# Kernel optimization log

Hardware: AMD Instinct MI355X
Metric: run time of the kernel (lower is better)

The kernel has to match this reference:

```python
import jax, jax.numpy as jnp
import numpy as np

N = 50000      # nodes
E = 800000     # random edges (self-loops added in reference, as PyG GATConv does)
G = 1024       # graphs in the batch
F_IN = 35      # num_features_xd
H1, C1 = 10, 35   # gcn1: heads=10, out=35 -> concat 350
H2, C2 = 1, 128   # gcn2: heads=1, out=128
NEG_SLOPE = 0.2   # PyG GATConv default leaky_relu slope


def setup_inputs() -> dict:
    key = jax.random.key(0)
    ks = jax.random.split(key, 16)
    g = lambda k, sh, fan: jax.random.normal(k, sh, jnp.float32) / jnp.sqrt(jnp.float32(fan))
    return {
        "x": jax.random.normal(ks[0], (N, F_IN), jnp.float32),
        "edge_index": jax.random.randint(ks[1], (2, E), 0, N),
        "batch": jnp.sort(jax.random.randint(ks[2], (N,), 0, G)),
        # gcn1 params
        "W1": g(ks[3], (F_IN, H1 * C1), F_IN),
        "att_src1": g(ks[4], (H1, C1), C1),
        "att_dst1": g(ks[5], (H1, C1), C1),
        "b1": jnp.zeros((H1 * C1,), jnp.float32),
        # gcn2 params
        "W2": g(ks[6], (H1 * C1, H2 * C2), H1 * C1),
        "att_src2": g(ks[7], (H2, C2), C2),
        "att_dst2": g(ks[8], (H2, C2), C2),
        "b2": jnp.zeros((H2 * C2,), jnp.float32),
        # dense head
        "Wg": g(ks[9], (C2, C2), C2),
        "bg": jnp.zeros((C2,), jnp.float32),
        "Wo": g(ks[10], (C2, 1), C2),
        "bo": jnp.zeros((1,), jnp.float32),
    }


def _gat_conv(x, src, dst, W, att_src, att_dst, b, heads, ch):
    """PyG GATConv (eval mode): edge attention + segment softmax + scatter sum."""
    h = (x @ W).reshape(-1, heads, ch)                      # [N,H,C]
    a_s = jnp.einsum('nhc,hc->nh', h, att_src)              # [N,H]
    a_d = jnp.einsum('nhc,hc->nh', h, att_dst)
    e = jax.nn.leaky_relu(a_s[src] + a_d[dst], NEG_SLOPE)   # [Etot,H]
    m = jax.ops.segment_max(e, dst, num_segments=N)         # segment softmax over dst
    ex = jnp.exp(e - m[dst])
    den = jax.ops.segment_sum(ex, dst, num_segments=N)
    alpha = ex / den[dst]                                   # [Etot,H]
    out = jax.ops.segment_sum(alpha[:, :, None] * h[src], dst, num_segments=N)
    return out.reshape(-1, heads * ch) + b                  # concat heads + bias


def reference(x, edge_index, batch, W1, att_src1, att_dst1, b1,
              W2, att_src2, att_dst2, b2, Wg, bg, Wo, bo):
    # add self-loops (PyG GATConv default add_self_loops=True)
    loop = jnp.arange(N, dtype=edge_index.dtype)
    src = jnp.concatenate([edge_index[0], loop])
    dst = jnp.concatenate([edge_index[1], loop])

    h = jax.nn.elu(_gat_conv(x, src, dst, W1, att_src1, att_dst1, b1, H1, C1))
    h = jax.nn.relu(_gat_conv(h, src, dst, W2, att_src2, att_dst2, b2, H2, C2))

    # global max pool over graphs
    pooled = jax.ops.segment_max(h, batch, num_segments=G)
    pooled = jnp.where(jnp.isneginf(pooled), 0.0, pooled)   # guard empty graphs

    z = jax.nn.relu(pooled @ Wg + bg)
    return z @ Wo + bo                                      # [G, 1]
```

## Files before the change

kernel.cpp:

```cpp
#include <hip/hip_runtime.h>
#include <hip/hip_bf16.h>
#include <cmath>

#define N_NODES 50000
#define N_EDGES 800000
#define N_GRAPHS 1024
#define F_IN 35
#define H1 10
#define C1 35
#define HC1 350
#define C2 128
#define NB256 196

typedef unsigned int uint32;
typedef __attribute__((ext_vector_type(8))) short short8;
typedef __attribute__((ext_vector_type(4))) float f32x4;

static __device__ __forceinline__ float bflo(uint32 u) { return __uint_as_float(u << 16); }
static __device__ __forceinline__ float bfhi(uint32 u) { return __uint_as_float(u & 0xffff0000u); }
static __device__ __forceinline__ unsigned short bfbits(float f) {
    return __builtin_bit_cast(unsigned short, __float2bfloat16(f));
}
static __device__ __forceinline__ uint32 packbf(float a, float b) {
    return ((uint32)bfbits(b) << 16) | (uint32)bfbits(a);
}
static __device__ __forceinline__ float lrelu(float e) { return (e > 0.f) ? e : 0.2f * e; }

__global__ void k_count(const int* __restrict__ dst, int* __restrict__ deg) {
    int e = blockIdx.x * blockDim.x + threadIdx.x;
    if (e < N_EDGES) atomicAdd(&deg[dst[e]], 1);
}

__global__ __launch_bounds__(256) void k_bsum(const int* __restrict__ deg, int* __restrict__ bsum) {
    const int i = blockIdx.x * 256 + threadIdx.x;
    int v = (i < N_NODES) ? deg[i] : 0;
#pragma unroll
    for (int off = 32; off; off >>= 1) v += __shfl_xor(v, off);
    __shared__ int ws[4];
    if ((threadIdx.x & 63) == 0) ws[threadIdx.x >> 6] = v;
    __syncthreads();
    if (threadIdx.x == 0) bsum[blockIdx.x] = ws[0] + ws[1] + ws[2] + ws[3];
}

__global__ __launch_bounds__(256) void k_bscan(const int* __restrict__ bsum, int* __restrict__ bpre) {
    __shared__ int buf[256];
    const int t = threadIdx.x;
    int v = (t < NB256) ? bsum[t] : 0;
    buf[t] = v;
    __syncthreads();
    for (int off = 1; off < 256; off <<= 1) {
        int u = (t >= off) ? buf[t - off] : 0;
        __syncthreads();
        buf[t] += u;
        __syncthreads();
    }
    if (t < NB256) bpre[t] = buf[t] - v;
}

__global__ __launch_bounds__(256) void k_boffs(const int* __restrict__ deg,
                                               const int* __restrict__ bpre,
                                               int* __restrict__ offs, int* __restrict__ cursor) {
    const int b = blockIdx.x, t = threadIdx.x;
    const int i = b * 256 + t;
    const int lane = t & 63, wid = t >> 6;
    int v = (i < N_NODES) ? deg[i] : 0;
    int s = v;
#pragma unroll
    for (int off = 1; off < 64; off <<= 1) {
        int u = __shfl_up(s, off);
        if (lane >= off) s += u;
    }
    __shared__ int wsum[4];
    if (lane == 63) wsum[wid] = s;
    __syncthreads();
    int wbase = 0;
    for (int w = 0; w < wid; ++w) wbase += wsum[w];
    int excl = bpre[b] + wbase + s - v;
    if (i < N_NODES) { offs[i] = excl; cursor[i] = excl; }
    if (i == 0) offs[N_NODES] = N_EDGES;
}

__global__ void k_fill(const int* __restrict__ src, const int* __restrict__ dst,
                       int* __restrict__ cursor, int* __restrict__ csr) {
    int e = blockIdx.x * blockDim.x + threadIdx.x;
    if (e < N_EDGES) {
        int p = atomicAdd(&cursor[dst[e]], 1);
        csr[p] = src[e];
    }
}

#define XBLK ((N_NODES * 8 + 255) / 256)
__global__ __launch_bounds__(256) void k_prep(const float* __restrict__ x,
                                              const float* __restrict__ W1,
                                              const float* __restrict__ attS1,
                                              const float* __restrict__ attD1,
                                              const float* __restrict__ W2,
                                              uint32* __restrict__ xbf,
                                              uint32* __restrict__ W1f,
                                              uint32* __restrict__ W2f) {
    const int b = blockIdx.x, t = threadIdx.x;
    if (b < XBLK) {
        int idx = b * 256 + t;
        if (idx >= N_NODES * 8) return;
        int n = idx >> 3, tt = idx & 7;
        uint32 o[4];
#pragma unroll
        for (int p = 0; p < 4; ++p) {
            int k0 = tt * 8 + 2 * p;
            float a = (k0 < F_IN) ? x[(size_t)n * F_IN + k0] : 0.f;
            float bb = (k0 + 1 < F_IN) ? x[(size_t)n * F_IN + k0 + 1] : 0.f;
            o[p] = packbf(a, bb);
        }
        uint32* d = xbf + (size_t)n * 32 + tt * 4;
        d[0] = o[0]; d[1] = o[1]; d[2] = o[2]; d[3] = o[3];
    } else if (b < XBLK + 12) {
        int idx = (b - XBLK) * 256 + t;
        if (idx >= 2 * 24 * 64) return;
        int lane = idx & 63;
        int tt = (idx >> 6) % 24;
        int kk = idx / (24 * 64);
        int c = tt * 16 + (lane & 15);
        int k0 = kk * 32 + (lane >> 4) * 8;
        uint32 o[4];
#pragma unroll
        for (int jj = 0; jj < 4; ++jj) {
            float v[2];
#pragma unroll
            for (int half = 0; half < 2; ++half) {
                int k = k0 + 2 * jj + half;
                float val = 0.f;
                if (k < F_IN) {
                    if (c < HC1) {
                        val = W1[k * HC1 + c];
                    } else if (c >= 352 && c < 362) {
                        int h = c - 352;
                        float s = 0.f;
                        for (int cc = 0; cc < C1; ++cc)
                            s = fmaf(W1[k * HC1 + h * C1 + cc], attS1[h * C1 + cc], s);
                        val = s;
                    } else if (c >= 368 && c < 378) {
                        int h = c - 368;
                        float s = 0.f;
                        for (int cc = 0; cc < C1; ++cc)
                            s = fmaf(W1[k * HC1 + h * C1 + cc], attD1[h * C1 + cc], s);
                        val = s;
                    }
                }
                v[half] = val;
            }
            o[jj] = packbf(v[0], v[1]);
        }
        uint32* d = W1f + (size_t)idx * 4;
        d[0] = o[0]; d[1] = o[1]; d[2] = o[2]; d[3] = o[3];
    } else {
        int idx = (b - XBLK - 12) * 256 + t;
        if (idx >= 11 * 8 * 64) return;
        int lane = idx & 63;
        int tt = (idx >> 6) & 7;
        int kk = idx >> 9;
        int c = tt * 16 + (lane & 15);
        int k0 = kk * 32 + (lane >> 4) * 8;
        uint32 o[4];
#pragma unroll
        for (int jj = 0; jj < 4; ++jj) {
            int ka = k0 + 2 * jj, kb = ka + 1;
            float va = (ka < HC1) ? W2[ka * C2 + c] : 0.f;
            float vb = (kb < HC1) ? W2[kb * C2 + c] : 0.f;
            o[jj] = packbf(va, vb);
        }
        uint32* d = W2f + (size_t)idx * 4;
        d[0] = o[0]; d[1] = o[1]; d[2] = o[2]; d[3] = o[3];
    }
}

__global__ __launch_bounds__(256) void k_gemm1(const short* __restrict__ xbf,
                                               const short8* __restrict__ W1f,
                                               unsigned short* __restrict__ h1b,
                                               float* __restrict__ a_s1,
                                               float* __restrict__ a_d1) {
    const int lane = threadIdx.x & 63;
    const int wid = threadIdx.x >> 6;
    const int mtile = blockIdx.x * 4 + wid;
    if (mtile >= N_NODES / 16) return;
    const int c_lo = lane & 15, grp = lane >> 4;
    const int m0 = mtile * 16;
    const short* aptr = xbf + (size_t)(m0 + c_lo) * 64 + grp * 8;

    f32x4 acc[24];
#pragma unroll
    for (int t = 0; t < 24; ++t) acc[t] = (f32x4){0.f, 0.f, 0.f, 0.f};
#pragma unroll
    for (int kk = 0; kk < 2; ++kk) {
        short8 a = *reinterpret_cast<const short8*>(aptr + kk * 32);
#pragma unroll
        for (int t = 0; t < 24; ++t) {
            short8 b = W1f[(kk * 24 + t) * 64 + lane];
            acc[t] = __builtin_amdgcn_mfma_f32_16x16x32_bf16(a, b, acc[t], 0, 0, 0);
        }
    }
#pragma unroll
    for (int r = 0; r < 4; ++r) {
        int node = m0 + grp * 4 + r;
#pragma unroll
        for (int t = 0; t < 22; ++t)
            h1b[(size_t)node * 352 + t * 16 + c_lo] = bfbits(acc[t][r]);
        if (c_lo < 10) {
            a_s1[node * 10 + c_lo] = acc[22][r];
            a_d1[node * 10 + c_lo] = acc[23][r];
        }
    }
}

__global__ __launch_bounds__(256) void k_agg1(const uint4* __restrict__ feat4,
                                              const float* __restrict__ a_s,
                                              const float* __restrict__ a_d,
                                              const int* __restrict__ offs,
                                              const int* __restrict__ csr,
                                              const float* __restrict__ bias,
                                              uint4* __restrict__ x2p4) {
    __shared__ float al[4][10][72];
    __shared__ float rdn[4][10];
    __shared__ int totmax[4];
    const int tid = threadIdx.x;
    const int lane = tid & 63, wid = tid >> 6;
    const int d = blockIdx.x * 4 + wid;
    const int o0 = offs[d];
    const int deg = offs[d + 1] - o0;
    const int total = deg + 1;
    const int cl = lane & 15, g = lane >> 4;

    if (lane < 8) {
#pragma unroll
        for (int h = 0; h < 10; ++h) al[wid][h][64 + lane] = 0.f;
    }
    if (lane == 0) totmax[wid] = total;
    __syncthreads();
    const int tmx = max(max(totmax[0], totmax[1]), max(totmax[2], totmax[3]));
    const int rounds = (tmx + 63) >> 6;

    float add[10];
    {
        const float2* ap = (const float2*)(a_d + (size_t)d * 10);
#pragma unroll
        for (int p = 0; p < 5; ++p) { float2 v = ap[p]; add[2 * p] = v.x; add[2 * p + 1] = v.y; }
    }
    const int u0 = cl, u1 = cl + 16, u2 = cl + 32;
    const bool has2 = (u2 < 44);
    const int hLo0 = (8 * u0) / 35, hHi0 = min((8 * u0 + 7) / 35, 9), bnd0 = 35 * hHi0;
    const int hLo1 = (8 * u1) / 35, hHi1 = min((8 * u1 + 7) / 35, 9), bnd1 = 35 * hHi1;
    const int hLo2 = has2 ? (8 * u2) / 35 : 0, hHi2 = has2 ? min((8 * u2 + 7) / 35, 9) : 0;
    const int bnd2 = 35 * hHi2;

    float acc0[8], acc1[8], acc2[8];
#pragma unroll
    for (int q = 0; q < 8; ++q) { acc0[q] = 0.f; acc1[q] = 0.f; acc2[q] = 0.f; }
    float den[10];
#pragma unroll
    for (int h = 0; h < 10; ++h) den[h] = 0.f;

    for (int rb = 0; rb < rounds; ++rb) {
        const int base = rb << 6;
        const int i = base + lane;
        int s_mine = d;
        if (i < total) {
            s_mine = (i < deg) ? csr[o0 + i] : d;
            const float2* ap = (const float2*)(a_s + (size_t)s_mine * 10);
            float2 v0 = ap[0], v1 = ap[1], v2 = ap[2], v3 = ap[3], v4 = ap[4];
            float e;
#define DOH(h, val)                            \
            e = __expf(lrelu((val) + add[h])); \
            den[h] += e;                       \
            al[wid][h][lane] = e;
            DOH(0, v0.x) DOH(1, v0.y) DOH(2, v1.x) DOH(3, v1.y) DOH(4, v2.x)
            DOH(5, v2.y) DOH(6, v3.x) DOH(7, v3.y) DOH(8, v4.x) DOH(9, v4.y)
#undef DOH
        } else {
#pragma unroll
            for (int h = 0; h < 10; ++h) al[wid][h][lane] = 0.f;
        }
        __syncthreads();
        const int cnt = min(64, total - base);
        if (cnt > 0) {
            int scur = __shfl(s_mine, g);
            uint4 v0 = feat4[(size_t)scur * 44 + u0];
            uint4 v1 = feat4[(size_t)scur * 44 + u1];
            uint4 v2 = has2 ? feat4[(size_t)scur * 44 + u2] : (uint4){0, 0, 0, 0};
            for (int jb = 0; jb < cnt; jb += 4) {
                uint4 w0 = v0, w1 = v1, w2 = v2;
                const int jj = jb + g;
                if (jb + 4 < cnt) {
                    int sn = __shfl(s_mine, jb + 4 + g);
                    v0 = feat4[(size_t)sn * 44 + u0];
                    v1 = feat4[(size_t)sn * 44 + u1];
                    if (has2) v2 = feat4[(size_t)sn * 44 + u2];
                }
#define ACCSLOT(ACC, W, HLO, HHI, BND, U)                                   \
                {                                                           \
                    float aLo = al[wid][HLO][jj], aHi = al[wid][HHI][jj];   \
                    _Pragma("unroll")                                       \
                    for (int q = 0; q < 4; ++q) {                           \
                        uint32 u = (q == 0) ? W.x : (q == 1) ? W.y : (q == 2) ? W.z : W.w; \
                        float aA = (8 * (U) + 2 * q >= (BND)) ? aHi : aLo;  \
                        float aB = (8 * (U) + 2 * q + 1 >= (BND)) ? aHi : aLo; \
                        ACC[2 * q] = fmaf(aA, bflo(u), ACC[2 * q]);         \
                        ACC[2 * q + 1] = fmaf(aB, bfhi(u), ACC[2 * q + 1]); \
                    }                                                       \
                }
                ACCSLOT(acc0, w0, hLo0, hHi0, bnd0, u0)
                ACCSLOT(acc1, w1, hLo1, hHi1, bnd1, u1)
                if (has2) ACCSLOT(acc2, w2, hLo2, hHi2, bnd2, u2)
#undef ACCSLOT
            }
        }
        __syncthreads();
    }
#pragma unroll
    for (int q = 0; q < 8; ++q) {
        acc0[q] += __shfl_xor(acc0[q], 16); acc0[q] += __shfl_xor(acc0[q], 32);
        acc1[q] += __shfl_xor(acc1[q], 16); acc1[q] += __shfl_xor(acc1[q], 32);
        acc2[q] += __shfl_xor(acc2[q], 16); acc2[q] += __shfl_xor(acc2[q], 32);
    }
#pragma unroll
    for (int off = 32; off > 0; off >>= 1) {
#pragma unroll
        for (int h = 0; h < 10; ++h) den[h] += __shfl_xor(den[h], off);
    }
    if (lane == 0) {
#pragma unroll
        for (int h = 0; h < 10; ++h) rdn[wid][h] = 1.f / den[h];
    }
    __syncthreads();
    if (g == 0) {
#define EPI(ACC, HLO, HHI, BND, U)                                          \
        {                                                                   \
            float rLo = rdn[wid][HLO], rHi = rdn[wid][HHI];                 \
            uint32 o[4];                                                    \
            _Pragma("unroll")                                               \
            for (int q = 0; q < 4; ++q) {                                   \
                int p = 4 * (U) + q;                                        \
                if (p < 175) {                                              \
                    int ch0 = 8 * (U) + 2 * q;                              \
                    float rA = (ch0 >= (BND)) ? rHi : rLo;                  \
                    float rB = (ch0 + 1 >= (BND)) ? rHi : rLo;              \
                    float v0 = ACC[2 * q] * rA + bias[ch0];                 \
                    float v1 = ACC[2 * q + 1] * rB + bias[ch0 + 1];         \
                    v0 = (v0 > 0.f) ? v0 : expm1f(v0);                      \
                    v1 = (v1 > 0.f) ? v1 : expm1f(v1);                      \
                    o[q] = packbf(v0, v1);                                  \
                } else {                                                    \
                    o[q] = 0u;                                              \
                }                                                           \
            }                                                               \
            uint4 ov = {o[0], o[1], o[2], o[3]};                            \
            x2p4[(size_t)d * 44 + (U)] = ov;                                \
        }
        EPI(acc0, hLo0, hHi0, bnd0, u0)
        EPI(acc1, hLo1, hHi1, bnd1, u1)
        if (has2) EPI(acc2, hLo2, hHi2, bnd2, u2)
#undef EPI
    }
}

__global__ __launch_bounds__(256) void k_gemm2(const short* __restrict__ x2p,
                                               const short8* __restrict__ W2f,
                                               const float* __restrict__ attS,
                                               const float* __restrict__ attD,
                                               unsigned short* __restrict__ h2b,
                                               float* __restrict__ a_s2, float* __restrict__ a_d2) {
    const int lane = threadIdx.x & 63;
    const int wid = threadIdx.x >> 6;
    const int mtile = blockIdx.x * 4 + wid;
    if (mtile >= N_NODES / 16) return;
    const int c_lo = lane & 15, grp = lane >> 4;
    const int m0 = mtile * 16;
    const short* aptr = x2p + (size_t)(m0 + c_lo) * 352 + grp * 8;

    f32x4 acc[8];
#pragma unroll
    for (int t = 0; t < 8; ++t) acc[t] = (f32x4){0.f, 0.f, 0.f, 0.f};
#pragma unroll
    for (int kk = 0; kk < 11; ++kk) {
        short8 a = *reinterpret_cast<const short8*>(aptr + kk * 32);
#pragma unroll
        for (int t = 0; t < 8; ++t) {
            short8 b = W2f[(kk * 8 + t) * 64 + lane];
            acc[t] = __builtin_amdgcn_mfma_f32_16x16x32_bf16(a, b, acc[t], 0, 0, 0);
        }
    }
    float attSv[8], attDv[8];
#pragma unroll
    for (int t = 0; t < 8; ++t) {
        attSv[t] = attS[t * 16 + c_lo];
        attDv[t] = attD[t * 16 + c_lo];
    }
    float ps[4] = {0, 0, 0, 0}, pd[4] = {0, 0, 0, 0};
#pragma unroll
    for (int t = 0; t < 8; ++t)
#pragma unroll
        for (int r = 0; r < 4; ++r) {
            ps[r] = fmaf(acc[t][r], attSv[t], ps[r]);
            pd[r] = fmaf(acc[t][r], attDv[t], pd[r]);
        }
#pragma unroll
    for (int r = 0; r < 4; ++r) {
        int node = m0 + grp * 4 + r;
#pragma unroll
        for (int t = 0; t < 8; ++t) h2b[(size_t)node * C2 + t * 16 + c_lo] = bfbits(acc[t][r]);
    }
#pragma unroll
    for (int r = 0; r < 4; ++r) {
        float s = ps[r], dd = pd[r];
#pragma unroll
        for (int off = 1; off < 16; off <<= 1) {
            s += __shfl_xor(s, off);
            dd += __shfl_xor(dd, off);
        }
        if (c_lo == 0) {
            int node = m0 + grp * 4 + r;
            a_s2[node] = s;
            a_d2[node] = dd;
        }
    }
}

__global__ __launch_bounds__(256) void k_agg2(const uint4* __restrict__ feat4,
                                              const float* __restrict__ a_s,
                                              const float* __restrict__ a_d,
                                              const int* __restrict__ offs,
                                              const int* __restrict__ csr,
                                              const float* __restrict__ b2,
                                              float* __restrict__ out2) {
    const int lane = threadIdx.x & 63;
    const int wid = threadIdx.x >> 6;
    const int d = blockIdx.x * 4 + wid;
    const int o0 = offs[d];
    const int deg = offs[d + 1] - o0;
    const int total = deg + 1;
    const float add = a_d[d];
    const int g = lane >> 4, cl = lane & 15;

    float acc[8];
#pragma unroll
    for (int q = 0; q < 8; ++q) acc[q] = 0.f;
    float den = 0.f;

    for (int base = 0; base < total; base += 64) {
        const int i = base + lane;
        int s_mine = d;
        float e_mine = 0.f;
        if (i < total) {
            s_mine = (i < deg) ? csr[o0 + i] : d;
            e_mine = __expf(lrelu(a_s[s_mine] + add));
            den += e_mine;
        }
        const int cnt = min(64, total - base);
        int sj = __shfl(s_mine, g);
        float aj = __shfl(e_mine, g);
        uint4 vc = feat4[(size_t)sj * 16 + cl];
        for (int jb = 0; jb < cnt; jb += 4) {
            uint4 v = vc;
            float a = aj;
            if (jb + 4 < cnt) {
                int ni = jb + 4 + g;
                int sn = __shfl(s_mine, ni);
                aj = __shfl(e_mine, ni);
                vc = feat4[(size_t)sn * 16 + cl];
            }
            acc[0] = fmaf(a, bflo(v.x), acc[0]);
            acc[1] = fmaf(a, bfhi(v.x), acc[1]);
            acc[2] = fmaf(a, bflo(v.y), acc[2]);
            acc[3] = fmaf(a, bfhi(v.y), acc[3]);
            acc[4] = fmaf(a, bflo(v.z), acc[4]);
            acc[5] = fmaf(a, bfhi(v.z), acc[5]);
            acc[6] = fmaf(a, bflo(v.w), acc[6]);
            acc[7] = fmaf(a, bfhi(v.w), acc[7]);
        }
    }
#pragma unroll
    for (int q = 0; q < 8; ++q) {
        acc[q] += __shfl_xor(acc[q], 16);
        acc[q] += __shfl_xor(acc[q], 32);
    }
#pragma unroll
    for (int off = 32; off > 0; off >>= 1) den += __shfl_xor(den, off);

    if (lane < 16) {
        const float rden = 1.f / den;
        const float4* bp = (const float4*)(b2 + 8 * cl);
        float4 b0 = bp[0], b1 = bp[1];
        float4 o0v, o1v;
        o0v.x = fmaxf(acc[0] * rden + b0.x, 0.f);
        o0v.y = fmaxf(acc[1] * rden + b0.y, 0.f);
        o0v.z = fmaxf(acc[2] * rden + b0.z, 0.f);
        o0v.w = fmaxf(acc[3] * rden + b0.w, 0.f);
        o1v.x = fmaxf(acc[4] * rden + b1.x, 0.f);
        o1v.y = fmaxf(acc[5] * rden + b1.y, 0.f);
        o1v.z = fmaxf(acc[6] * rden + b1.z, 0.f);
        o1v.w = fmaxf(acc[7] * rden + b1.w, 0.f);
        float4* op = (float4*)(out2 + (size_t)d * C2 + 8 * cl);
        op[0] = o0v;
        op[1] = o1v;
    }
}

__global__ __launch_bounds__(128) void k_pool(const float* __restrict__ out2,
                                              const int* __restrict__ batch,
                                              float* __restrict__ pooled) {
    const int c = threadIdx.x;
    const int n0 = blockIdx.x * 50;
    const int n1 = min(n0 + 50, N_NODES);
    int curB = batch[n0];
    float curM = 0.f;
    float v = out2[(size_t)n0 * C2 + c];
    for (int n = n0; n < n1; ++n) {
        float cur = v;
        int b = batch[n];
        if (n + 1 < n1) v = out2[(size_t)(n + 1) * C2 + c];
        if (b != curB) {
            atomicMax((int*)&pooled[curB * C2 + c], __float_as_int(curM));
            curB = b;
            curM = cur;
        } else {
            curM = fmaxf(curM, cur);
        }
    }
    atomicMax((int*)&pooled[curB * C2 + c], __float_as_int(curM));
}

__global__ __launch_bounds__(128) void k_head(const float* __restrict__ pooled,
                                              const float* __restrict__ Wg,
                                              const float* __restrict__ bg,
                                              const float* __restrict__ Wo,
                                              const float* __restrict__ bo,
                                              float* __restrict__ out) {
    __shared__ float p[C2];
    __shared__ float wsum[2];
    const int g = blockIdx.x;
    const int tid = threadIdx.x;
    p[tid] = pooled[g * C2 + tid];
    __syncthreads();
    float acc = bg[tid];
#pragma unroll 8
    for (int k = 0; k < C2; ++k) acc = fmaf(p[k], Wg[k * C2 + tid], acc);
    float z = fmaxf(acc, 0.f);
    float prod = z * Wo[tid];
#pragma unroll
    for (int off = 32; off; off >>= 1) prod += __shfl_down(prod, off);
    if ((tid & 63) == 0) wsum[tid >> 6] = prod;
    __syncthreads();
    if (tid == 0) out[g] = wsum[0] + wsum[1] + bo[0];
}

extern "C" void kernel_launch(void* const* d_in, const int* in_sizes, int n_in,
                              void* d_out, int out_size, void* d_ws, size_t ws_size,
                              hipStream_t stream) {
    const float* x        = (const float*)d_in[0];
    const int*   ei       = (const int*)d_in[1];
    const int*   batch    = (const int*)d_in[2];
    const float* W1       = (const float*)d_in[3];
    const float* att_src1 = (const float*)d_in[4];
    const float* att_dst1 = (const float*)d_in[5];
    const float* b1       = (const float*)d_in[6];
    const float* W2       = (const float*)d_in[7];
    const float* att_src2 = (const float*)d_in[8];
    const float* att_dst2 = (const float*)d_in[9];
    const float* b2       = (const float*)d_in[10];
    const float* Wg       = (const float*)d_in[11];
    const float* bg       = (const float*)d_in[12];
    const float* Wo       = (const float*)d_in[13];
    const float* bo       = (const float*)d_in[14];
    const int* src = ei;
    const int* dst = ei + N_EDGES;

    char* ws = (char*)d_ws;
    size_t off = 0;
    auto alloc = [&](size_t bytes) -> char* {
        char* p = ws + off;
        off = (off + bytes + 255) & ~(size_t)255;
        return p;
    };
    int*    deg    = (int*)alloc((size_t)N_NODES * 4);
    int*    offs   = (int*)alloc((size_t)(N_NODES + 1) * 4);
    int*    cursor = (int*)alloc((size_t)N_NODES * 4);
    int*    csr    = (int*)alloc((size_t)N_EDGES * 4);
    int*    bsum   = (int*)alloc((size_t)NB256 * 4);
    int*    bpre   = (int*)alloc((size_t)NB256 * 4);
    float*  a_s1   = (float*)alloc((size_t)N_NODES * H1 * 4);
    float*  a_d1   = (float*)alloc((size_t)N_NODES * H1 * 4);
    float*  a_s2   = (float*)alloc((size_t)N_NODES * 4);
    float*  a_d2   = (float*)alloc((size_t)N_NODES * 4);
    float*  pooled = (float*)alloc((size_t)N_GRAPHS * C2 * 4);
    uint32* xbf    = (uint32*)alloc((size_t)N_NODES * 32 * 4);
    unsigned short* h1b = (unsigned short*)alloc((size_t)N_NODES * 352 * 2);
    uint32* x2p    = (uint32*)alloc((size_t)N_NODES * 176 * 4);
    unsigned short* h2b = (unsigned short*)alloc((size_t)N_NODES * C2 * 2);
    uint32* W1f    = (uint32*)alloc((size_t)2 * 24 * 64 * 16);
    uint32* W2f    = (uint32*)alloc((size_t)11 * 8 * 64 * 16);
    float*  out2   = (float*)h1b;

    hipMemsetAsync(deg, 0, (size_t)N_NODES * 4, stream);
    hipMemsetAsync(pooled, 0, (size_t)N_GRAPHS * C2 * 4, stream);

    k_count<<<(N_EDGES + 255) / 256, 256, 0, stream>>>(dst, deg);
    k_bsum<<<NB256, 256, 0, stream>>>(deg, bsum);
    k_bscan<<<1, 256, 0, stream>>>(bsum, bpre);
    k_boffs<<<NB256, 256, 0, stream>>>(deg, bpre, offs, cursor);
    k_fill<<<(N_EDGES + 255) / 256, 256, 0, stream>>>(src, dst, cursor, csr);

    k_prep<<<XBLK + 34, 256, 0, stream>>>(x, W1, att_src1, att_dst1, W2, xbf, W1f, W2f);

    k_gemm1<<<(N_NODES / 16 + 3) / 4, 256, 0, stream>>>((const short*)xbf, (const short8*)W1f,
                                                        h1b, a_s1, a_d1);

    k_agg1<<<N_NODES / 4, 256, 0, stream>>>((const uint4*)h1b, a_s1, a_d1, offs, csr, b1,
                                            (uint4*)x2p);

    k_gemm2<<<(N_NODES / 16 + 3) / 4, 256, 0, stream>>>((const short*)x2p, (const short8*)W2f,
                                                        att_src2, att_dst2, h2b, a_s2, a_d2);

    k_agg2<<<N_NODES / 4, 256, 0, stream>>>((const uint4*)h2b, a_s2, a_d2, offs, csr, b2, out2);

    k_pool<<<(N_NODES + 49) / 50, 128, 0, stream>>>(out2, batch, pooled);

    k_head<<<N_GRAPHS, 128, 0, stream>>>(pooled, Wg, bg, Wo, bo, (float*)d_out);
}
```

Measured before the change: 402.4 us.

## Aggregate raw 35-dim inputs per head before layer-1 projection

Layer 1 now uses linearity: instead of projecting every node to 350 channels and then gathering 352-wide bf16 rows per edge, it gathers the 40-wide padded input rows, weights them with per-head attention, and applies the per-head W1 projection afterwards with MFMA. A constant-one input channel carries the bias through the GEMM, and the softmax denominator comes from the aggregated bias channel. Attention logits are computed separately through folded W1·att vectors. This cuts per-edge gather traffic, but it adds a 10×40-per-node intermediate buffer, a larger post-aggregation GEMM, and extra kernels, and it adds occupancy hints.

```diff
diff --git a/kernel.cpp b/kernel.cpp
--- a/kernel.cpp
+++ b/kernel.cpp
@@ -89,36 +89,51 @@
     }
 }
 
-#define XBLK ((N_NODES * 8 + 255) / 256)
+#define XB ((N_NODES * 5 + 255) / 256)
 __global__ __launch_bounds__(256) void k_prep(const float* __restrict__ x,
                                               const float* __restrict__ W1,
                                               const float* __restrict__ attS1,
                                               const float* __restrict__ attD1,
+                                              const float* __restrict__ b1,
                                               const float* __restrict__ W2,
                                               uint32* __restrict__ xbf,
-                                              uint32* __restrict__ W1f,
+                                              float* __restrict__ fold,
+                                              uint32* __restrict__ W1g,
                                               uint32* __restrict__ W2f) {
     const int b = blockIdx.x, t = threadIdx.x;
-    if (b < XBLK) {
+    if (b < XB) {
         int idx = b * 256 + t;
-        if (idx >= N_NODES * 8) return;
-        int n = idx >> 3, tt = idx & 7;
+        if (idx >= N_NODES * 5) return;
+        int n = idx / 5, s = idx - n * 5;
         uint32 o[4];
 #pragma unroll
         for (int p = 0; p < 4; ++p) {
-            int k0 = tt * 8 + 2 * p;
-            float a = (k0 < F_IN) ? x[(size_t)n * F_IN + k0] : 0.f;
-            float bb = (k0 + 1 < F_IN) ? x[(size_t)n * F_IN + k0 + 1] : 0.f;
+            int ch0 = s * 8 + 2 * p, ch1 = ch0 + 1;
+            float a = (ch0 < F_IN) ? x[(size_t)n * F_IN + ch0] : (ch0 == 35 ? 1.f : 0.f);
+            float bb = (ch1 < F_IN) ? x[(size_t)n * F_IN + ch1] : (ch1 == 35 ? 1.f : 0.f);
             o[p] = packbf(a, bb);
         }
-        uint32* d = xbf + (size_t)n * 32 + tt * 4;
+        uint32* d = xbf + (size_t)idx * 4;
         d[0] = o[0]; d[1] = o[1]; d[2] = o[2]; d[3] = o[3];
-    } else if (b < XBLK + 12) {
-        int idx = (b - XBLK) * 256 + t;
-        if (idx >= 2 * 24 * 64) return;
+    } else if (b < XB + 3) {
+        int idx = (b - XB) * 256 + t;
+        if (idx >= 700) return;
+        int k = idx / 20, o = idx - k * 20;
+        int h = (o < 10) ? o : o - 10;
+        const float* att = (o < 10) ? attS1 : attD1;
+        float s = 0.f;
+        for (int c = 0; c < C1; ++c)
+            s = fmaf(W1[k * HC1 + h * C1 + c], att[h * C1 + c], s);
+        fold[k * 20 + o] = s;
+    } else if (b < XB + 3 + 15) {
+        int idx = (b - XB - 3) * 256 + t;
+        if (idx >= 10 * 2 * 3 * 64) return;
         int lane = idx & 63;
-        int tt = (idx >> 6) % 24;
-        int kk = idx / (24 * 64);
+        int rest = idx >> 6;
+        int tt = rest % 3;
+        int rest2 = rest / 3;
+        int kk = rest2 & 1;
+        int h = rest2 >> 1;
         int c = tt * 16 + (lane & 15);
         int k0 = kk * 32 + (lane >> 4) * 8;
         uint32 o[4];
@@ -129,31 +144,18 @@
             for (int half = 0; half < 2; ++half) {
                 int k = k0 + 2 * jj + half;
                 float val = 0.f;
-                if (k < F_IN) {
-                    if (c < HC1) {
-                        val = W1[k * HC1 + c];
-                    } else if (c >= 352 && c < 362) {
-                        int h = c - 352;
-                        float s = 0.f;
-                        for (int cc = 0; cc < C1; ++cc)
-                            s = fmaf(W1[k * HC1 + h * C1 + cc], attS1[h * C1 + cc], s);
-                        val = s;
-                    } else if (c >= 368 && c < 378) {
-                        int h = c - 368;
-                        float s = 0.f;
-                        for (int cc = 0; cc < C1; ++cc)
-                            s = fmaf(W1[k * HC1 + h * C1 + cc], attD1[h * C1 + cc], s);
-                        val = s;
-                    }
+                if (c < C1) {
+                    if (k < F_IN) val = W1[k * HC1 + h * C1 + c];
+                    else if (k == 35) val = b1[h * C1 + c];
                 }
                 v[half] = val;
             }
             o[jj] = packbf(v[0], v[1]);
         }
-        uint32* d = W1f + (size_t)idx * 4;
+        uint32* d = W1g + (size_t)idx * 4;
         d[0] = o[0]; d[1] = o[1]; d[2] = o[2]; d[3] = o[3];
     } else {
-        int idx = (b - XBLK - 12) * 256 + t;
+        int idx = (b - XB - 3 - 15) * 256 + t;
         if (idx >= 11 * 8 * 64) return;
         int lane = idx & 63;
         int tt = (idx >> 6) & 7;
@@ -173,192 +175,173 @@
     }
 }
 
-__global__ __launch_bounds__(256) void k_gemm1(const short* __restrict__ xbf,
-                                               const short8* __restrict__ W1f,
-                                               unsigned short* __restrict__ h1b,
-                                               float* __restrict__ a_s1,
-                                               float* __restrict__ a_d1) {
+__global__ __launch_bounds__(256) void k_att1(const float* __restrict__ x,
+                                              const float* __restrict__ fold,
+                                              float* __restrict__ a_s1,
+                                              float* __restrict__ a_d1) {
+    int idx = blockIdx.x * 256 + threadIdx.x;
+    if (idx >= N_NODES * 20) return;
+    int n = idx / 20, o = idx - n * 20;
+    const float* xr = x + (size_t)n * F_IN;
+    float acc = 0.f;
+#pragma unroll
+    for (int k = 0; k < F_IN; ++k) acc = fmaf(xr[k], fold[k * 20 + o], acc);
+    if (o < 10) a_s1[n * 10 + o] = acc;
+    else        a_d1[n * 10 + (o - 10)] = acc;
+}
+
+__global__ __launch_bounds__(256, 8) void k_aggx(const uint4* __restrict__ xbf4,
+                                                 const float* __restrict__ a_s,
+                                                 const float* __restrict__ a_d,
+                                                 const int* __restrict__ offs,
+                                                 const int* __restrict__ csr,
+                                                 uint4* __restrict__ aggx4) {
+    __shared__ float al[4][10][68];
+    __shared__ float addl[4][10];
+    __shared__ int totmax[4];
+    const int tid = threadIdx.x, lane = tid & 63, wid = tid >> 6;
+    const int d = blockIdx.x * 4 + wid;
+    const int o0 = offs[d];
+    const int deg = offs[d + 1] - o0;
+    const int total = deg + 1;
+    const int g = lane >> 4, u = lane & 15;
+    const int hg = (u >= 10) ? 2 : ((u >= 5) ? 1 : 0);
+    const int sl = u - hg * 5;
+    const bool act = (u < 15);
+    const int h0 = hg * 4;
+
+    if (lane < 10) addl[wid][lane] = a_d[(size_t)d * 10 + lane];
+    if (lane < 4) {
+#pragma unroll
+        for (int h = 0; h < 10; ++h) al[wid][h][64 + lane] = 0.f;
+    }
+    if (lane == 0) totmax[wid] = total;
+    __syncthreads();
+    const int tmx = max(max(totmax[0], totmax[1]), max(totmax[2], totmax[3]));
+    const int rounds = (tmx + 63) >> 6;
+
+    float acc[4][8];
+#pragma unroll
+    for (int a = 0; a < 4; ++a)
+#pragma unroll
+        for (int q = 0; q < 8; ++q) acc[a][q] = 0.f;
+
+    for (int rb = 0; rb < rounds; ++rb) {
+        const int base = rb << 6;
+        const int i = base + lane;
+        int s_mine = d;
+        if (i < total) {
+            if (i < deg) s_mine = csr[o0 + i];
+            const float2* ap = (const float2*)(a_s + (size_t)s_mine * 10);
+            float2 p0 = ap[0], p1 = ap[1], p2 = ap[2], p3 = ap[3], p4 = ap[4];
+            al[wid][0][lane] = __expf(lrelu(p0.x + addl[wid][0]));
+            al[wid][1][lane] = __expf(lrelu(p0.y + addl[wid][1]));
+            al[wid][2][lane] = __expf(lrelu(p1.x + addl[wid][2]));
+            al[wid][3][lane] = __expf(lrelu(p1.y + addl[wid][3]));
+            al[wid][4][lane] = __expf(lrelu(p2.x + addl[wid][4]));
+            al[wid][5][lane] = __expf(lrelu(p2.y + addl[wid][5]));
+            al[wid][6][lane] = __expf(lrelu(p3.x + addl[wid][6]));
+            al[wid][7][lane] = __expf(lrelu(p3.y + addl[wid][7]));
+            al[wid][8][lane] = __expf(lrelu(p4.x + addl[wid][8]));
+            al[wid][9][lane] = __expf(lrelu(p4.y + addl[wid][9]));
+        } else {
+#pragma unroll
+            for (int h = 0; h < 10; ++h) al[wid][h][lane] = 0.f;
+        }
+        __syncthreads();
+        const int cnt = min(64, total - base);
+        if (cnt > 0) {
+            int scur = __shfl(s_mine, g);
+            uint4 v = act ? xbf4[(size_t)scur * 5 + sl] : (uint4){0, 0, 0, 0};
+            for (int jb = 0; jb < cnt; jb += 4) {
+                uint4 w = v;
+                const int jj = jb + g;
+                if (jb + 4 < cnt) {
+                    int sn = __shfl(s_mine, jb + 4 + g);
+                    if (act) v = xbf4[(size_t)sn * 5 + sl];
+                }
+                float f0 = bflo(w.x), f1 = bfhi(w.x), f2 = bflo(w.y), f3 = bfhi(w.y);
+                float f4 = bflo(w.z), f5 = bfhi(w.z), f6 = bflo(w.w), f7 = bfhi(w.w);
+#pragma unroll
+                for (int a = 0; a < 4; ++a) {
+                    const int hidx = min(h0 + a, 9);
+                    const float aj = al[wid][hidx][jj];
+                    acc[a][0] = fmaf(aj, f0, acc[a][0]);
+                    acc[a][1] = fmaf(aj, f1, acc[a][1]);
+                    acc[a][2] = fmaf(aj, f2, acc[a][2]);
+                    acc[a][3] = fmaf(aj, f3, acc[a][3]);
+                    acc[a][4] = fmaf(aj, f4, acc[a][4]);
+                    acc[a][5] = fmaf(aj, f5, acc[a][5]);
+                    acc[a][6] = fmaf(aj, f6, acc[a][6]);
+                    acc[a][7] = fmaf(aj, f7, acc[a][7]);
+                }
+            }
+        }
+        __syncthreads();
+    }
+#pragma unroll
+    for (int a = 0; a < 4; ++a)
+#pragma unroll
+        for (int q = 0; q < 8; ++q) {
+            acc[a][q] += __shfl_xor(acc[a][q], 16);
+            acc[a][q] += __shfl_xor(acc[a][q], 32);
+        }
+    const int nh = (hg == 2) ? 2 : 4;
+#pragma unroll
+    for (int a = 0; a < 4; ++a) {
+        float den = __shfl(acc[a][3], hg * 5 + 4);
+        float rdn = 1.f / den;
+        if (g == 0 && act && a < nh) {
+            uint32 o[4];
+#pragma unroll
+            for (int q = 0; q < 4; ++q)
+                o[q] = packbf(acc[a][2 * q] * rdn, acc[a][2 * q + 1] * rdn);
+            uint4 ov = {o[0], o[1], o[2], o[3]};
+            aggx4[((size_t)d * 10 + h0 + a) * 5 + sl] = ov;
+        }
+    }
+}
+
+__global__ __launch_bounds__(256, 8) void k_gemm1b(const short* __restrict__ aggx,
+                                                   const short8* __restrict__ W1g,
+                                                   unsigned short* __restrict__ x2p) {
     const int lane = threadIdx.x & 63;
     const int wid = threadIdx.x >> 6;
     const int mtile = blockIdx.x * 4 + wid;
     if (mtile >= N_NODES / 16) return;
     const int c_lo = lane & 15, grp = lane >> 4;
     const int m0 = mtile * 16;
-    const short* aptr = xbf + (size_t)(m0 + c_lo) * 64 + grp * 8;
-
-    f32x4 acc[24];
-#pragma unroll
-    for (int t = 0; t < 24; ++t) acc[t] = (f32x4){0.f, 0.f, 0.f, 0.f};
-#pragma unroll
-    for (int kk = 0; kk < 2; ++kk) {
-        short8 a = *reinterpret_cast<const short8*>(aptr + kk * 32);
-#pragma unroll
-        for (int t = 0; t < 24; ++t) {
-            short8 b = W1f[(kk * 24 + t) * 64 + lane];
-            acc[t] = __builtin_amdgcn_mfma_f32_16x16x32_bf16(a, b, acc[t], 0, 0, 0);
-        }
-    }
-#pragma unroll
-    for (int r = 0; r < 4; ++r) {
-        int node = m0 + grp * 4 + r;
-#pragma unroll
-        for (int t = 0; t < 22; ++t)
-            h1b[(size_t)node * 352 + t * 16 + c_lo] = bfbits(acc[t][r]);
-        if (c_lo < 10) {
-            a_s1[node * 10 + c_lo] = acc[22][r];
-            a_d1[node * 10 + c_lo] = acc[23][r];
-        }
-    }
-}
-
-__global__ __launch_bounds__(256) void k_agg1(const uint4* __restrict__ feat4,
-                                              const float* __restrict__ a_s,
-                                              const float* __restrict__ a_d,
-                                              const int* __restrict__ offs,
-                                              const int* __restrict__ csr,
-                                              const float* __restrict__ bias,
-                                              uint4* __restrict__ x2p4) {
-    __shared__ float al[4][10][72];
-    __shared__ float rdn[4][10];
-    __shared__ int totmax[4];
-    const int tid = threadIdx.x;
-    const int lane = tid & 63, wid = tid >> 6;
-    const int d = blockIdx.x * 4 + wid;
-    const int o0 = offs[d];
-    const int deg = offs[d + 1] - o0;
-    const int total = deg + 1;
-    const int cl = lane & 15, g = lane >> 4;
-
-    if (lane < 8) {
-#pragma unroll
-        for (int h = 0; h < 10; ++h) al[wid][h][64 + lane] = 0.f;
-    }
-    if (lane == 0) totmax[wid] = total;
-    __syncthreads();
-    const int tmx = max(max(totmax[0], totmax[1]), max(totmax[2], totmax[3]));
-    const int rounds = (tmx + 63) >> 6;
-
-    float add[10];
-    {
-        const float2* ap = (const float2*)(a_d + (size_t)d * 10);
-#pragma unroll
-        for (int p = 0; p < 5; ++p) { float2 v = ap[p]; add[2 * p] = v.x; add[2 * p + 1] = v.y; }
-    }
-    const int u0 = cl, u1 = cl + 16, u2 = cl + 32;
-    const bool has2 = (u2 < 44);
-    const int hLo0 = (8 * u0) / 35, hHi0 = min((8 * u0 + 7) / 35, 9), bnd0 = 35 * hHi0;
-    const int hLo1 = (8 * u1) / 35, hHi1 = min((8 * u1 + 7) / 35, 9), bnd1 = 35 * hHi1;
-    const int hLo2 = has2 ? (8 * u2) / 35 : 0, hHi2 = has2 ? min((8 * u2 + 7) / 35, 9) : 0;
-    const int bnd2 = 35 * hHi2;
-
-    float acc0[8], acc1[8], acc2[8];
-#pragma unroll
-    for (int q = 0; q < 8; ++q) { acc0[q] = 0.f; acc1[q] = 0.f; acc2[q] = 0.f; }
-    float den[10];
-#pragma unroll
-    for (int h = 0; h < 10; ++h) den[h] = 0.f;
-
-    for (int rb = 0; rb < rounds; ++rb) {
-        const int base = rb << 6;
-        const int i = base + lane;
-        int s_mine = d;
-        if (i < total) {
-            s_mine = (i < deg) ? csr[o0 + i] : d;
-            const float2* ap = (const float2*)(a_s + (size_t)s_mine * 10);
-            float2 v0 = ap[0], v1 = ap[1], v2 = ap[2], v3 = ap[3], v4 = ap[4];
-            float e;
-#define DOH(h, val)                            \
-            e = __expf(lrelu((val) + add[h])); \
-            den[h] += e;                       \
-            al[wid][h][lane] = e;
-            DOH(0, v0.x) DOH(1, v0.y) DOH(2, v1.x) DOH(3, v1.y) DOH(4, v2.x)
-            DOH(5, v2.y) DOH(6, v3.x) DOH(7, v3.y) DOH(8, v4.x) DOH(9, v4.y)
-#undef DOH
-        } else {
-#pragma unroll
-            for (int h = 0; h < 10; ++h) al[wid][h][lane] = 0.f;
-        }
-        __syncthreads();
-        const int cnt = min(64, total - base);
-        if (cnt > 0) {
-            int scur = __shfl(s_mine, g);
-            uint4 v0 = feat4[(size_t)scur * 44 + u0];
-            uint4 v1 = feat4[(size_t)scur * 44 + u1];
-            uint4 v2 = has2 ? feat4[(size_t)scur * 44 + u2] : (uint4){0, 0, 0, 0};
-            for (int jb = 0; jb < cnt; jb += 4) {
-                uint4 w0 = v0, w1 = v1, w2 = v2;
-                const int jj = jb + g;
-                if (jb + 4 < cnt) {
-                    int sn = __shfl(s_mine, jb + 4 + g);
-                    v0 = feat4[(size_t)sn * 44 + u0];
-                    v1 = feat4[(size_t)sn * 44 + u1];
-                    if (has2) v2 = feat4[(size_t)sn * 44 + u2];
+    const size_t abase = (size_t)(m0 + c_lo) * 400 + grp * 8;
+
+#pragma unroll
+    for (int h = 0; h < 10; ++h) {
+        const short* ap = aggx + abase + h * 40;
+        short8 a0 = *reinterpret_cast<const short8*>(ap);
+        short8 a1 = *reinterpret_cast<const short8*>(ap + 32);
+        f32x4 acc[3];
+#pragma unroll
+        for (int tt = 0; tt < 3; ++tt) acc[tt] = (f32x4){0.f, 0.f, 0.f, 0.f};
+#pragma unroll
+        for (int tt = 0; tt < 3; ++tt)
+            acc[tt] = __builtin_amdgcn_mfma_f32_16x16x32_bf16(a0, W1g[((h * 2 + 0) * 3 + tt) * 64 + lane], acc[tt], 0, 0, 0);
+#pragma unroll
+        for (int tt = 0; tt < 3; ++tt)
+            acc[tt] = __builtin_amdgcn_mfma_f32_16x16x32_bf16(a1, W1g[((h * 2 + 1) * 3 + tt) * 64 + lane], acc[tt], 0, 0, 0);
+#pragma unroll
+        for (int tt = 0; tt < 3; ++tt) {
+            int c = tt * 16 + c_lo;
+            if (c < C1) {
+#pragma unroll
+                for (int r = 0; r < 4; ++r) {
+                    int node = m0 + grp * 4 + r;
+                    float v = acc[tt][r];
+                    v = (v > 0.f) ? v : expm1f(v);
+                    x2p[(size_t)node * 352 + h * C1 + c] = bfbits(v);
                 }
-#define ACCSLOT(ACC, W, HLO, HHI, BND, U)                                   \
-                {                                                           \
-                    float aLo = al[wid][HLO][jj], aHi = al[wid][HHI][jj];   \
-                    _Pragma("unroll")                                       \
-                    for (int q = 0; q < 4; ++q) {                           \
-                        uint32 u = (q == 0) ? W.x : (q == 1) ? W.y : (q == 2) ? W.z : W.w; \
-                        float aA = (8 * (U) + 2 * q >= (BND)) ? aHi : aLo;  \
-                        float aB = (8 * (U) + 2 * q + 1 >= (BND)) ? aHi : aLo; \
-                        ACC[2 * q] = fmaf(aA, bflo(u), ACC[2 * q]);         \
-                        ACC[2 * q + 1] = fmaf(aB, bfhi(u), ACC[2 * q + 1]); \
-                    }                                                       \
-                }
-                ACCSLOT(acc0, w0, hLo0, hHi0, bnd0, u0)
-                ACCSLOT(acc1, w1, hLo1, hHi1, bnd1, u1)
-                if (has2) ACCSLOT(acc2, w2, hLo2, hHi2, bnd2, u2)
-#undef ACCSLOT
             }
         }
-        __syncthreads();
-    }
-#pragma unroll
-    for (int q = 0; q < 8; ++q) {
-        acc0[q] += __shfl_xor(acc0[q], 16); acc0[q] += __shfl_xor(acc0[q], 32);
-        acc1[q] += __shfl_xor(acc1[q], 16); acc1[q] += __shfl_xor(acc1[q], 32);
-        acc2[q] += __shfl_xor(acc2[q], 16); acc2[q] += __shfl_xor(acc2[q], 32);
-    }
-#pragma unroll
-    for (int off = 32; off > 0; off >>= 1) {
-#pragma unroll
-        for (int h = 0; h < 10; ++h) den[h] += __shfl_xor(den[h], off);
-    }
-    if (lane == 0) {
-#pragma unroll
-        for (int h = 0; h < 10; ++h) rdn[wid][h] = 1.f / den[h];
-    }
-    __syncthreads();
-    if (g == 0) {
-#define EPI(ACC, HLO, HHI, BND, U)                                          \
-        {                                                                   \
-            float rLo = rdn[wid][HLO], rHi = rdn[wid][HHI];                 \
-            uint32 o[4];                                                    \
-            _Pragma("unroll")                                               \
-            for (int q = 0; q < 4; ++q) {                                   \
-                int p = 4 * (U) + q;                                        \
-                if (p < 175) {                                              \
-                    int ch0 = 8 * (U) + 2 * q;                              \
-                    float rA = (ch0 >= (BND)) ? rHi : rLo;                  \
-                    float rB = (ch0 + 1 >= (BND)) ? rHi : rLo;              \
-                    float v0 = ACC[2 * q] * rA + bias[ch0];                 \
-                    float v1 = ACC[2 * q + 1] * rB + bias[ch0 + 1];         \
-                    v0 = (v0 > 0.f) ? v0 : expm1f(v0);                      \
-                    v1 = (v1 > 0.f) ? v1 : expm1f(v1);                      \
-                    o[q] = packbf(v0, v1);                                  \
-                } else {                                                    \
-                    o[q] = 0u;                                              \
-                }                                                           \
-            }                                                               \
-            uint4 ov = {o[0], o[1], o[2], o[3]};                            \
-            x2p4[(size_t)d * 44 + (U)] = ov;                                \
-        }
-        EPI(acc0, hLo0, hHi0, bnd0, u0)
-        EPI(acc1, hLo1, hHi1, bnd1, u1)
-        if (has2) EPI(acc2, hLo2, hHi2, bnd2, u2)
-#undef EPI
-    }
+    }
+    if (lane < 16) ((uint32*)x2p)[(size_t)(m0 + lane) * 176 + 175] = 0u;
 }
 
 __global__ __launch_bounds__(256) void k_gemm2(const short* __restrict__ x2p,
@@ -423,13 +406,13 @@
     }
 }
 
-__global__ __launch_bounds__(256) void k_agg2(const uint4* __restrict__ feat4,
-                                              const float* __restrict__ a_s,
-                                              const float* __restrict__ a_d,
-                                              const int* __restrict__ offs,
-                                              const int* __restrict__ csr,
-                                              const float* __restrict__ b2,
-                                              float* __restrict__ out2) {
+__global__ __launch_bounds__(256, 8) void k_agg2(const uint4* __restrict__ feat4,
+                                                 const float* __restrict__ a_s,
+                                                 const float* __restrict__ a_d,
+                                                 const int* __restrict__ offs,
+                                                 const int* __restrict__ csr,
+                                                 const float* __restrict__ b2,
+                                                 float* __restrict__ out2) {
     const int lane = threadIdx.x & 63;
     const int wid = threadIdx.x >> 6;
     const int d = blockIdx.x * 4 + wid;
@@ -590,13 +573,14 @@
     float*  a_s2   = (float*)alloc((size_t)N_NODES * 4);
     float*  a_d2   = (float*)alloc((size_t)N_NODES * 4);
     float*  pooled = (float*)alloc((size_t)N_GRAPHS * C2 * 4);
-    uint32* xbf    = (uint32*)alloc((size_t)N_NODES * 32 * 4);
-    unsigned short* h1b = (unsigned short*)alloc((size_t)N_NODES * 352 * 2);
+    float*  fold   = (float*)alloc((size_t)700 * 4);
+    uint32* xbf    = (uint32*)alloc((size_t)N_NODES * 20 * 4);
+    short*  aggx   = (short*)alloc((size_t)N_NODES * 400 * 2 + 256);
     uint32* x2p    = (uint32*)alloc((size_t)N_NODES * 176 * 4);
     unsigned short* h2b = (unsigned short*)alloc((size_t)N_NODES * C2 * 2);
-    uint32* W1f    = (uint32*)alloc((size_t)2 * 24 * 64 * 16);
+    uint32* W1g    = (uint32*)alloc((size_t)10 * 2 * 3 * 64 * 16);
     uint32* W2f    = (uint32*)alloc((size_t)11 * 8 * 64 * 16);
-    float*  out2   = (float*)h1b;
+    float*  out2   = (float*)aggx;
 
     hipMemsetAsync(deg, 0, (size_t)N_NODES * 4, stream);
     hipMemsetAsync(pooled, 0, (size_t)N_GRAPHS * C2 * 4, stream);
@@ -607,13 +591,15 @@
     k_boffs<<<NB256, 256, 0, stream>>>(deg, bpre, offs, cursor);
     k_fill<<<(N_EDGES + 255) / 256, 256, 0, stream>>>(src, dst, cursor, csr);
 
-    k_prep<<<XBLK + 34, 256, 0, stream>>>(x, W1, att_src1, att_dst1, W2, xbf, W1f, W2f);
-
-    k_gemm1<<<(N_NODES / 16 + 3) / 4, 256, 0, stream>>>((const short*)xbf, (const short8*)W1f,
-                                                        h1b, a_s1, a_d1);
-
-    k_agg1<<<N_NODES / 4, 256, 0, stream>>>((const uint4*)h1b, a_s1, a_d1, offs, csr, b1,
-                                            (uint4*)x2p);
+    k_prep<<<XB + 3 + 15 + 22, 256, 0, stream>>>(x, W1, att_src1, att_dst1, b1, W2,
+                                                 xbf, fold, W1g, W2f);
+    k_att1<<<(N_NODES * 20 + 255) / 256, 256, 0, stream>>>(x, fold, a_s1, a_d1);
+
+    k_aggx<<<N_NODES / 4, 256, 0, stream>>>((const uint4*)xbf, a_s1, a_d1, offs, csr,
+                                            (uint4*)aggx);
+
+    k_gemm1b<<<(N_NODES / 16 + 3) / 4, 256, 0, stream>>>(aggx, (const short8*)W1g,
+                                                         (unsigned short*)x2p);
 
     k_gemm2<<<(N_NODES / 16 + 3) / 4, 256, 0, stream>>>((const short*)x2p, (const short8*)W2f,
                                                         att_src2, att_dst2, h2b, a_s2, a_d2);
```

Measured after the change: 349.0 us. 13.3% less time.
